# Kernel tuning notes

Measured on AMD Instinct MI355X. Metric: run time of the kernel, lower is better.

## Reference

```python
import jax, jax.numpy as jnp
import numpy as np

N = 100_000      # lidar points (KITTI-scale)
E = 800_000      # knn edges, avg degree 8
C_IN = 4
INTERNAL_H, INTERNAL_W = 240, 1216   # INTERNAL_IMG_SIZE


def setup_inputs() -> dict:
    key = jax.random.key(0)
    ks = jax.random.split(key, 16)
    x = jax.random.normal(ks[0], (N, C_IN), jnp.float32)
    # lidar-like points in velodyne frame: x fwd [5,70], y left [-20,20], z up [-2,1]
    u = jax.random.uniform(ks[1], (N, 3), jnp.float32)
    pos = jnp.stack([5.0 + 65.0 * u[:, 0],
                     -20.0 + 40.0 * u[:, 1],
                     -2.0 + 3.0 * u[:, 2]], axis=1)
    edge_index = jax.random.randint(ks[2], (2, E), 0, N, dtype=jnp.int32)
    batch = jnp.zeros((N,), jnp.int32)
    # folded calibration P2 @ R0 @ Tr: pinhole cam looking down velodyne +x
    f, cx, cy = 720.0, 621.0, 250.0
    proj = jnp.array([[cx, -f, 0.0, 0.0],
                      [cy, 0.0, -f, 0.0],
                      [1.0, 0.0, 0.0, 0.0]], jnp.float32)
    dims = [(C_IN + 3, 64), (64 + 3, 128), (128 + 3, 256)]
    params = {}
    ki = 3
    for li, (din, dout) in enumerate(dims, 1):
        s1, s2 = 1.0 / np.sqrt(din), 1.0 / np.sqrt(dout)
        params[f"w1_{li}"] = jax.random.uniform(ks[ki], (din, dout), jnp.float32, -s1, s1); ki += 1
        params[f"b1_{li}"] = jnp.zeros((dout,), jnp.float32)
        params[f"w2_{li}"] = jax.random.uniform(ks[ki], (dout, dout), jnp.float32, -s2, s2); ki += 1
        params[f"b2_{li}"] = jnp.zeros((dout,), jnp.float32)
    return dict(x=x, pos=pos, edge_index=edge_index, batch=batch, proj=proj,
                img_h=375, img_w=1242, **params)


def _pointnet_conv(x, pos, src, dst, w1, b1, w2, b2):
    # message: local_nn([x_j, pos_j - pos_i]) with MLP = lin1 -> relu -> lin2; aggr = max
    m = jnp.concatenate([x[src], pos[src] - pos[dst]], axis=1)     # [E', din]
    h = jnp.maximum(m @ w1 + b1, 0.0) @ w2 + b2                    # [E', dout]
    return jax.ops.segment_max(h, dst, num_segments=x.shape[0])


def reference(x, pos, edge_index, batch, proj, img_h, img_w,
              w1_1, b1_1, w2_1, b2_1,
              w1_2, b1_2, w2_2, b2_2,
              w1_3, b1_3, w2_3, b2_3):
    n = x.shape[0]
    # PointNetConv adds self-loops by default -> every segment non-empty
    loops = jnp.arange(n, dtype=edge_index.dtype)
    src = jnp.concatenate([edge_index[0], loops])
    dst = jnp.concatenate([edge_index[1], loops])

    h = _pointnet_conv(x, pos, src, dst, w1_1, b1_1, w2_1, b2_1)   # [N, 64]
    h = _pointnet_conv(h, pos, src, dst, w1_2, b1_2, w2_2, b2_2)   # [N, 128]
    h = _pointnet_conv(h, pos, src, dst, w1_3, b1_3, w2_3, b2_3)   # [N, 256]

    # projection: (proj @ [pos; 1]) -> [3, N]; perspective divide; int16 trunc
    hom = proj @ jnp.concatenate([pos.T, jnp.ones((1, n), pos.dtype)], axis=0)
    off_u, off_v = img_w - INTERNAL_W, img_h - INTERNAL_H
    ui = (hom[0] / hom[2]).astype(jnp.int16).astype(jnp.int32) - off_u
    vi = (hom[1] / hom[2]).astype(jnp.int16).astype(jnp.int32) - off_v
    valid = (ui >= 0) & (vi >= 0) & (ui < INTERNAL_W) & (vi < INTERNAL_H)
    # route invalid points out-of-bounds so mode='drop' discards them
    ui = jnp.where(valid, ui, INTERNAL_W)
    vi = jnp.where(valid, vi, INTERNAL_H)

    img = jnp.zeros((1, h.shape[1], INTERNAL_W, INTERNAL_H), h.dtype)  # (B=1, C, 1216, 240)
    img = img.at[0, :, ui, vi].add(h, mode='drop')

    # max_pool2d(kernel=4, stride=4) -> (1, 256, 304, 60)
    B, C, W, H = img.shape
    pooled = img.reshape(B, C, W // 4, 4, H // 4, 4).max(axis=(3, 5))
    return pooled
```

## Files before the change

kernel.cpp:

```cpp
#include <hip/hip_runtime.h>
#include <cstdint>

#define N_PTS 100000
#define N_EDGE 800000
#define N_ITEMS (N_EDGE + N_PTS)
#define IMG_W 1216
#define IMG_H 240
#define OW 304
#define OH 60
#define CHUNK 32
#define BIN_BLOCKS 391

typedef _Float16 f16;
typedef _Float16 f16x8 __attribute__((ext_vector_type(8)));
typedef float f32x4 __attribute__((ext_vector_type(4)));

__device__ __forceinline__ void atomicMaxF(float* addr, float v) {
    if (v >= 0.0f) atomicMax((int*)addr, __float_as_int(v));
    else atomicMin((unsigned int*)addr, __float_as_uint(v));
}

__global__ __launch_bounds__(256)
void init_out_kernel(float* __restrict__ p, long n)
{
    long i = ((long)blockIdx.x * 256 + threadIdx.x) * 4;
    if (i < n) {
        float4 v = {-INFINITY, -INFINITY, -INFINITY, -INFINITY};
        *(float4*)&p[i] = v;
    }
}

template<int DX, int KP, int D>
__global__ __launch_bounds__(256)
void node_mfma_kernel(const float* __restrict__ X, const float* __restrict__ pos,
                      const f16* __restrict__ w1t, const float* __restrict__ b1,
                      f16* __restrict__ A)
{
    constexpr int KB = KP / 32;
    constexpr int NB = D / 16;
    const int tid = threadIdx.x;
    const int wave = tid >> 6;
    const int lane = tid & 63;
    const int row = lane & 15;
    const int kg = lane >> 4;
    const int wbase = (blockIdx.x * 4 + wave) * 32;

    f16x8 pa[2][KB];
#pragma unroll
    for (int mh = 0; mh < 2; ++mh) {
        int n = wbase + mh * 16 + row;
        int ns = (n < N_PTS) ? n : 0;
#pragma unroll
        for (int kb = 0; kb < KB; ++kb) {
            const int c0 = kb * 32 + kg * 8;
            f16x8 h;
#pragma unroll
            for (int j = 0; j < 8; ++j) {
                int k = c0 + j;
                float v = 0.0f;
                if (k < DX) v = X[(long)ns * DX + k];
                else if (k < DX + 3) v = pos[(long)ns * 3 + (k - DX)];
                h[j] = (f16)v;
            }
            pa[mh][kb] = h;
        }
    }

#pragma unroll 2
    for (int nb = 0; nb < NB; ++nb) {
        f32x4 acc0 = {0.0f, 0.0f, 0.0f, 0.0f};
        f32x4 acc1 = {0.0f, 0.0f, 0.0f, 0.0f};
#pragma unroll
        for (int kb = 0; kb < KB; ++kb) {
            f16x8 pb = *(const f16x8*)&w1t[(long)(nb * 16 + row) * KP + kb * 32 + kg * 8];
            acc0 = __builtin_amdgcn_mfma_f32_16x16x32_f16(pa[0][kb], pb, acc0, 0, 0, 0);
            acc1 = __builtin_amdgcn_mfma_f32_16x16x32_f16(pa[1][kb], pb, acc1, 0, 0, 0);
        }
        const int col = nb * 16 + row;
        const float bb = b1[col];
#pragma unroll
        for (int reg = 0; reg < 4; ++reg) {
            int r = kg * 4 + reg;
            int n0 = wbase + r;
            int n1 = wbase + 16 + r;
            if (n0 < N_PTS) A[(long)n0 * D + col] = (f16)(acc0[reg] + bb);
            if (n1 < N_PTS) A[(long)n1 * D + col] = (f16)(acc1[reg] + bb);
        }
    }
}

__global__ void cvt_w1(const float* __restrict__ w1, f16* __restrict__ w1t,
                       int K, int KP, int D)
{
    int i = blockIdx.x * 256 + threadIdx.x;
    if (i >= D * KP) return;
    int c = i / KP, k = i % KP;
    w1t[i] = (k < K) ? (f16)w1[k * D + c] : (f16)0.0f;
}

__global__ void cvt_w2(const float* __restrict__ w2, f16* __restrict__ w2t, int D)
{
    int i = blockIdx.x * 256 + threadIdx.x;
    if (i >= D * D) return;
    int n = i / D, k = i % D;
    w2t[i] = (f16)w2[k * D + n];
}

__global__ void init_hist_kernel(int* __restrict__ hist)
{
    int i = blockIdx.x * 256 + threadIdx.x;
    if (i < N_PTS) hist[i] = 1;
}

__global__ void hist_kernel(const int* __restrict__ ei, int* __restrict__ hist)
{
    int e = blockIdx.x * 256 + threadIdx.x;
    if (e < N_EDGE) atomicAdd(&hist[ei[N_EDGE + e]], 1);
}

__global__ void bsum_kernel(const int* __restrict__ hist, int* __restrict__ bsum)
{
    __shared__ int s[256];
    int i = blockIdx.x * 256 + threadIdx.x;
    s[threadIdx.x] = (i < N_PTS) ? hist[i] : 0;
    __syncthreads();
    for (int off = 128; off > 0; off >>= 1) {
        if (threadIdx.x < off) s[threadIdx.x] += s[threadIdx.x + off];
        __syncthreads();
    }
    if (threadIdx.x == 0) bsum[blockIdx.x] = s[0];
}

__global__ void scan_bsum_kernel(int* __restrict__ bsum)
{
    __shared__ int s[512];
    int t = threadIdx.x;
    int v = (t < BIN_BLOCKS) ? bsum[t] : 0;
    s[t] = v;
    __syncthreads();
    for (int off = 1; off < 512; off <<= 1) {
        int u = (t >= off) ? s[t - off] : 0;
        __syncthreads();
        s[t] += u;
        __syncthreads();
    }
    if (t < BIN_BLOCKS) bsum[t] = s[t] - v;
}

__global__ void rowptr_kernel(const int* __restrict__ hist, const int* __restrict__ bsum,
                              int* __restrict__ woff)
{
    __shared__ int s[256];
    int i = blockIdx.x * 256 + threadIdx.x;
    int v = (i < N_PTS) ? hist[i] : 0;
    s[threadIdx.x] = v;
    __syncthreads();
    for (int off = 1; off < 256; off <<= 1) {
        int u = (threadIdx.x >= off) ? s[threadIdx.x - off] : 0;
        __syncthreads();
        s[threadIdx.x] += u;
        __syncthreads();
    }
    if (i < N_PTS) woff[i] = bsum[blockIdx.x] + s[threadIdx.x] - v;
}

__global__ void scatter_edges_kernel(const int* __restrict__ ei, int* __restrict__ woff,
                                     int* __restrict__ srcS, int* __restrict__ dstS)
{
    int e = blockIdx.x * 256 + threadIdx.x;
    if (e >= N_ITEMS) return;
    int s, d;
    if (e < N_EDGE) { s = ei[e]; d = ei[N_EDGE + e]; }
    else            { s = d = e - N_EDGE; }
    int p = atomicAdd(&woff[d], 1);
    srcS[p] = s;
    dstS[p] = d;
}

template<int D>
__global__ __launch_bounds__(256)
void gemm_msg_kernel(const int* __restrict__ srcA, const int* __restrict__ dstA,
                     const f16* __restrict__ A, const float* __restrict__ pos,
                     const float* __restrict__ w1p, const f16* __restrict__ w2t,
                     const float* __restrict__ b2, float* __restrict__ OUT, int nItems)
{
    constexpr int KB = D / 32;
    constexpr int NB = D / 16;
    const int tid = threadIdx.x;
    const int wave = tid >> 6;
    const int lane = tid & 63;
    const int row = lane & 15;
    const int kg = lane >> 4;
    const long wbase = ((long)blockIdx.x * 4 + wave) * 32;

    int s[2], d[2];
    float px[2], py[2], pz[2];
#pragma unroll
    for (int mh = 0; mh < 2; ++mh) {
        long e = wbase + mh * 16 + row;
        bool ok = (e < nItems);
        int ss = ok ? srcA[e] : 0;
        int dd = ok ? dstA[e] : -1;
        s[mh] = ss; d[mh] = dd;
        int dsafe = ok ? dd : 0;
        px[mh] = pos[(long)dsafe * 3 + 0];
        py[mh] = pos[(long)dsafe * 3 + 1];
        pz[mh] = pos[(long)dsafe * 3 + 2];
    }

    f16x8 pa[2][KB];
#pragma unroll
    for (int kb = 0; kb < KB; ++kb) {
        const int c0 = kb * 32 + kg * 8;
        f16x8 a0 = *(const f16x8*)&A[(long)s[0] * D + c0];
        f16x8 a1 = *(const f16x8*)&A[(long)s[1] * D + c0];
        f16x8 h0, h1;
#pragma unroll
        for (int j = 0; j < 8; ++j) {
            float wx = w1p[c0 + j];
            float wy = w1p[D + c0 + j];
            float wz = w1p[2 * D + c0 + j];
            h0[j] = (f16)fmaxf((float)a0[j] - (px[0] * wx + py[0] * wy + pz[0] * wz), 0.0f);
            h1[j] = (f16)fmaxf((float)a1[j] - (px[1] * wx + py[1] * wy + pz[1] * wz), 0.0f);
        }
        pa[0][kb] = h0;
        pa[1][kb] = h1;
    }

    int dd0[4], dd1[4];
#pragma unroll
    for (int reg = 0; reg < 4; ++reg) {
        int r = kg * 4 + reg;
        dd0[reg] = __shfl(d[0], r);
        dd1[reg] = __shfl(d[1], r);
    }
    const bool a01 = (dd0[1] == dd0[0]), a12 = (dd0[2] == dd0[1]), a23 = (dd0[3] == dd0[2]);
    const bool b01 = (dd1[1] == dd1[0]), b12 = (dd1[2] == dd1[1]), b23 = (dd1[3] == dd1[2]);
    const bool aAll = a01 && a12 && a23, bAll = b01 && b12 && b23;
    const int aN0 = __shfl(dd0[0], lane + 16);
    const int bN0 = __shfl(dd1[0], lane + 16);
    const int aFn = __shfl((int)aAll, lane + 16);
    const int bFn = __shfl((int)bAll, lane + 16);
    const bool aCo = (kg < 3) && (dd0[3] == aN0);
    const bool bCo = (kg < 3) && (dd1[3] == bN0);
    const int lprev = (lane >= 16) ? (lane - 16) : 0;
    const int aP3 = __shfl(dd0[3], lprev);
    const int bP3 = __shfl(dd1[3], lprev);
    const bool aHd = (kg == 0) || (dd0[0] != aP3);
    const bool bHd = (kg == 0) || (dd1[0] != bP3);

#pragma unroll
    for (int nb = 0; nb < NB; ++nb) {
        f32x4 acc0 = {0.0f, 0.0f, 0.0f, 0.0f};
        f32x4 acc1 = {0.0f, 0.0f, 0.0f, 0.0f};
#pragma unroll
        for (int kb = 0; kb < KB; ++kb) {
            f16x8 pb = *(const f16x8*)&w2t[(long)(nb * 16 + row) * D + kb * 32 + kg * 8];
            acc0 = __builtin_amdgcn_mfma_f32_16x16x32_f16(pa[0][kb], pb, acc0, 0, 0, 0);
            acc1 = __builtin_amdgcn_mfma_f32_16x16x32_f16(pa[1][kb], pb, acc1, 0, 0, 0);
        }
        const int col = nb * 16 + row;
        const float bb = b2[col];
        {
            const float v0 = acc0[0] + bb, v1 = acc0[1] + bb, v2 = acc0[2] + bb, v3 = acc0[3] + bb;
            const float s3 = v3;
            const float s2 = a23 ? fmaxf(v2, s3) : v2;
            const float s1 = a12 ? fmaxf(v1, s2) : v1;
            const float s0 = a01 ? fmaxf(v0, s1) : v0;
            float P = v0;
            P = a01 ? fmaxf(P, v1) : P;
            P = (a01 && a12) ? fmaxf(P, v2) : P;
            P = aAll ? fmaxf(P, v3) : P;
            float T = -INFINITY;
#pragma unroll
            for (int it = 0; it < 3; ++it) {
                float Pn = __shfl(P, lane + 16);
                float Tn = __shfl(T, lane + 16);
                T = aCo ? fmaxf(Pn, aFn ? Tn : -INFINITY) : T;
            }
            const float x0 = aAll ? fmaxf(s0, T) : s0;
            const float x1 = (a12 && a23) ? fmaxf(s1, T) : s1;
            const float x2 = a23 ? fmaxf(s2, T) : s2;
            const float x3 = fmaxf(s3, T);
            if (aHd  && dd0[0] >= 0) atomicMaxF(&OUT[(long)dd0[0] * D + col], x0);
            if (!a01 && dd0[1] >= 0) atomicMaxF(&OUT[(long)dd0[1] * D + col], x1);
            if (!a12 && dd0[2] >= 0) atomicMaxF(&OUT[(long)dd0[2] * D + col], x2);
            if (!a23 && dd0[3] >= 0) atomicMaxF(&OUT[(long)dd0[3] * D + col], x3);
        }
        {
            const float v0 = acc1[0] + bb, v1 = acc1[1] + bb, v2 = acc1[2] + bb, v3 = acc1[3] + bb;
            const float s3 = v3;
            const float s2 = b23 ? fmaxf(v2, s3) : v2;
            const float s1 = b12 ? fmaxf(v1, s2) : v1;
            const float s0 = b01 ? fmaxf(v0, s1) : v0;
            float P = v0;
            P = b01 ? fmaxf(P, v1) : P;
            P = (b01 && b12) ? fmaxf(P, v2) : P;
            P = bAll ? fmaxf(P, v3) : P;
            float T = -INFINITY;
#pragma unroll
            for (int it = 0; it < 3; ++it) {
                float Pn = __shfl(P, lane + 16);
                float Tn = __shfl(T, lane + 16);
                T = bCo ? fmaxf(Pn, bFn ? Tn : -INFINITY) : T;
            }
            const float x0 = bAll ? fmaxf(s0, T) : s0;
            const float x1 = (b12 && b23) ? fmaxf(s1, T) : s1;
            const float x2 = b23 ? fmaxf(s2, T) : s2;
            const float x3 = fmaxf(s3, T);
            if (bHd  && dd1[0] >= 0) atomicMaxF(&OUT[(long)dd1[0] * D + col], x0);
            if (!b01 && dd1[1] >= 0) atomicMaxF(&OUT[(long)dd1[1] * D + col], x1);
            if (!b12 && dd1[2] >= 0) atomicMaxF(&OUT[(long)dd1[2] * D + col], x2);
            if (!b23 && dd1[3] >= 0) atomicMaxF(&OUT[(long)dd1[3] * D + col], x3);
        }
    }
}

__global__ void proj_kernel(const float* __restrict__ pos, const float* __restrict__ proj,
                            const int* __restrict__ img_h, const int* __restrict__ img_w,
                            int* __restrict__ pix)
{
    int n = blockIdx.x * blockDim.x + threadIdx.x;
    if (n >= N_PTS) return;
    float px = pos[n * 3 + 0], py = pos[n * 3 + 1], pz = pos[n * 3 + 2];
    float h0 = proj[0] * px + proj[1] * py + proj[2]  * pz + proj[3];
    float h1 = proj[4] * px + proj[5] * py + proj[6]  * pz + proj[7];
    float h2 = proj[8] * px + proj[9] * py + proj[10] * pz + proj[11];
    int off_u = img_w[0] - IMG_W;
    int off_v = img_h[0] - IMG_H;
    int ui = (int)(short)(h0 / h2) - off_u;
    int vi = (int)(short)(h1 / h2) - off_v;
    bool valid = (ui >= 0) && (vi >= 0) && (ui < IMG_W) && (vi < IMG_H);
    pix[n] = valid ? (ui * IMG_H + vi) : -1;
}

__global__ __launch_bounds__(256)
void scatter_kernel(const float* __restrict__ H, const int* __restrict__ pix,
                    float* __restrict__ img, int cbase)
{
    long g = (long)blockIdx.x * blockDim.x + threadIdx.x;
    if (g >= (long)N_PTS * CHUNK) return;
    int n = (int)(g / CHUNK);
    int c = (int)(g % CHUNK);
    int p = pix[n];
    if (p < 0) return;
    atomicAdd(&img[(long)p * CHUNK + c], H[(long)n * 256 + cbase + c]);
}

__global__ __launch_bounds__(CHUNK)
void pool_kernel(const float* __restrict__ img, float* __restrict__ out, int cbase)
{
    int cell = blockIdx.x;
    int wc = cell / OH, hc = cell % OH;
    int c = threadIdx.x;
    float mx = -INFINITY;
#pragma unroll
    for (int i = 0; i < 4; ++i)
#pragma unroll
        for (int j = 0; j < 4; ++j) {
            long p = (long)(wc * 4 + i) * IMG_H + (hc * 4 + j);
            mx = fmaxf(mx, img[p * CHUNK + c]);
        }
    out[(long)(cbase + c) * (OW * OH) + wc * OH + hc] = mx;
}

extern "C" void kernel_launch(void* const* d_in, const int* in_sizes, int n_in,
                              void* d_out, int out_size, void* d_ws, size_t ws_size,
                              hipStream_t stream)
{
    const float* x     = (const float*)d_in[0];
    const float* pos   = (const float*)d_in[1];
    const int*   ei    = (const int*)d_in[2];
    const float* proj  = (const float*)d_in[4];
    const int*   img_h = (const int*)d_in[5];
    const int*   img_w = (const int*)d_in[6];
    const float* w1_1 = (const float*)d_in[7];
    const float* b1_1 = (const float*)d_in[8];
    const float* w2_1 = (const float*)d_in[9];
    const float* b2_1 = (const float*)d_in[10];
    const float* w1_2 = (const float*)d_in[11];
    const float* b1_2 = (const float*)d_in[12];
    const float* w2_2 = (const float*)d_in[13];
    const float* b2_2 = (const float*)d_in[14];
    const float* w1_3 = (const float*)d_in[15];
    const float* b1_3 = (const float*)d_in[16];
    const float* w2_3 = (const float*)d_in[17];
    const float* b2_3 = (const float*)d_in[18];
    float* out = (float*)d_out;

    if (ws_size < 162400000ull) return;
    char* ws = (char*)d_ws;
    float* HH   = (float*)(ws + 0);
    float* F1   = (float*)(ws + 0);
    float* F0   = (float*)(ws + 51200000);
    f16*   A12  = (f16*)(ws + 76800000);
    f16*   A3   = (f16*)(ws + 102400000);
    float* img  = (float*)(ws + 102400000);
    int*   pix  = (int*)(ws + 153600000);
    f16*   w2t3 = (f16*)(ws + 154000000);
    f16*   w2t2 = (f16*)(ws + 154131072);
    f16*   w2t1 = (f16*)(ws + 154163840);
    int*   srcS = (int*)(ws + 154200000);
    int*   dstS = (int*)(ws + 157800000);
    int*   hist = (int*)(ws + 161400000);
    int*   woff = (int*)(ws + 161800000);
    int*   bsum = (int*)(ws + 162200000);
    f16*   w1t3 = (f16*)(ws + 162210000);
    f16*   w1t2 = (f16*)(ws + 162300000);
    f16*   w1t1 = (f16*)(ws + 162330000);

    const int NODE_BLOCKS = (N_PTS + 127) / 128;
    const int EDGE_BLOCKS = (N_ITEMS + 127) / 128;
    const int E256  = (N_EDGE + 255) / 256;
    const int I256  = (N_ITEMS + 255) / 256;

    init_hist_kernel<<<BIN_BLOCKS, 256, 0, stream>>>(hist);
    hist_kernel<<<E256, 256, 0, stream>>>(ei, hist);
    bsum_kernel<<<BIN_BLOCKS, 256, 0, stream>>>(hist, bsum);
    scan_bsum_kernel<<<1, 512, 0, stream>>>(bsum);
    rowptr_kernel<<<BIN_BLOCKS, 256, 0, stream>>>(hist, bsum, woff);
    scatter_edges_kernel<<<I256, 256, 0, stream>>>(ei, woff, srcS, dstS);

    cvt_w1<<<(64 * 32 + 255) / 256, 256, 0, stream>>>(w1_1, w1t1, 7, 32, 64);
    cvt_w1<<<(128 * 96 + 255) / 256, 256, 0, stream>>>(w1_2, w1t2, 67, 96, 128);
    cvt_w1<<<(256 * 160 + 255) / 256, 256, 0, stream>>>(w1_3, w1t3, 131, 160, 256);
    cvt_w2<<<(64 * 64 + 255) / 256, 256, 0, stream>>>(w2_1, w2t1, 64);
    cvt_w2<<<(128 * 128 + 255) / 256, 256, 0, stream>>>(w2_2, w2t2, 128);
    cvt_w2<<<(256 * 256 + 255) / 256, 256, 0, stream>>>(w2_3, w2t3, 256);
    proj_kernel<<<(N_PTS + 255) / 256, 256, 0, stream>>>(pos, proj, img_h, img_w, pix);
    init_out_kernel<<<(N_PTS * 64 / 4 + 255) / 256, 256, 0, stream>>>(F0, (long)N_PTS * 64);
    init_out_kernel<<<(N_PTS * 128 / 4 + 255) / 256, 256, 0, stream>>>(F1, (long)N_PTS * 128);

    node_mfma_kernel<4, 32, 64><<<NODE_BLOCKS, 256, 0, stream>>>(x, pos, w1t1, b1_1, A12);
    gemm_msg_kernel<64><<<EDGE_BLOCKS, 256, 0, stream>>>(srcS, dstS, A12, pos, w1_1 + 4 * 64, w2t1, b2_1, F0, N_ITEMS);

    node_mfma_kernel<64, 96, 128><<<NODE_BLOCKS, 256, 0, stream>>>(F0, pos, w1t2, b1_2, A12);
    gemm_msg_kernel<128><<<EDGE_BLOCKS, 256, 0, stream>>>(srcS, dstS, A12, pos, w1_2 + 64 * 128, w2t2, b2_2, F1, N_ITEMS);

    node_mfma_kernel<128, 160, 256><<<NODE_BLOCKS, 256, 0, stream>>>(F1, pos, w1t3, b1_3, A3);
    init_out_kernel<<<(N_PTS * 256 / 4 + 255) / 256, 256, 0, stream>>>(HH, (long)N_PTS * 256);
    gemm_msg_kernel<256><<<EDGE_BLOCKS, 256, 0, stream>>>(srcS, dstS, A3, pos, w1_3 + 128 * 256, w2t3, b2_3, HH, N_ITEMS);

    for (int cb = 0; cb < 256; cb += CHUNK) {
        hipMemsetAsync(img, 0, (size_t)IMG_W * IMG_H * CHUNK * 4, stream);
        scatter_kernel<<<(N_PTS * CHUNK) / 256, 256, 0, stream>>>(HH, pix, img, cb);
        pool_kernel<<<OW * OH, CHUNK, 0, stream>>>(img, out, cb);
    }
}
```

Before: 1.735 ms.

## Use 16-edge-per-wave MFMA message kernel for layer 3

Adds a variant of the edge message kernel where each wave handles 16 edges instead of 32, keeping the first-layer activations in registers and running 16x16x32 MFMAs over the 256-wide output. It is used only for the third PointNet layer, where the D=256 tile likely causes register pressure and low occupancy. The trade is more blocks and twice as many loads of W2 per edge, in exchange for fewer registers per wave and possibly higher occupancy.

```diff
diff --git a/kernel.cpp b/kernel.cpp
--- a/kernel.cpp
+++ b/kernel.cpp
@@ -313,6 +313,96 @@
             if (!b12 && dd1[2] >= 0) atomicMaxF(&OUT[(long)dd1[2] * D + col], x2);
             if (!b23 && dd1[3] >= 0) atomicMaxF(&OUT[(long)dd1[3] * D + col], x3);
         }
+    }
+}
+
+template<int D>
+__global__ __launch_bounds__(256)
+void gemm_msg16_kernel(const int* __restrict__ srcA, const int* __restrict__ dstA,
+                       const f16* __restrict__ A, const float* __restrict__ pos,
+                       const float* __restrict__ w1p, const f16* __restrict__ w2t,
+                       const float* __restrict__ b2, float* __restrict__ OUT, int nItems)
+{
+    constexpr int KB = D / 32;
+    constexpr int NB = D / 16;
+    const int tid = threadIdx.x;
+    const int wave = tid >> 6;
+    const int lane = tid & 63;
+    const int row = lane & 15;
+    const int kg = lane >> 4;
+    const long wbase = ((long)blockIdx.x * 4 + wave) * 16;
+
+    const long e = wbase + row;
+    const bool ok = (e < nItems);
+    const int ss = ok ? srcA[e] : 0;
+    const int dd = ok ? dstA[e] : -1;
+    const int dsafe = ok ? dd : 0;
+    const float px = pos[(long)dsafe * 3 + 0];
+    const float py = pos[(long)dsafe * 3 + 1];
+    const float pz = pos[(long)dsafe * 3 + 2];
+
+    f16x8 pa[KB];
+#pragma unroll
+    for (int kb = 0; kb < KB; ++kb) {
+        const int c0 = kb * 32 + kg * 8;
+        f16x8 a = *(const f16x8*)&A[(long)ss * D + c0];
+        f16x8 h;
+#pragma unroll
+        for (int j = 0; j < 8; ++j) {
+            float wx = w1p[c0 + j];
+            float wy = w1p[D + c0 + j];
+            float wz = w1p[2 * D + c0 + j];
+            h[j] = (f16)fmaxf((float)a[j] - (px * wx + py * wy + pz * wz), 0.0f);
+        }
+        pa[kb] = h;
+    }
+
+    int dd0[4];
+#pragma unroll
+    for (int reg = 0; reg < 4; ++reg) dd0[reg] = __shfl(dd, kg * 4 + reg);
+    const bool a01 = (dd0[1] == dd0[0]), a12 = (dd0[2] == dd0[1]), a23 = (dd0[3] == dd0[2]);
+    const bool aAll = a01 && a12 && a23;
+    const int aN0 = __shfl(dd0[0], lane + 16);
+    const int aFn = __shfl((int)aAll, lane + 16);
+    const bool aCo = (kg < 3) && (dd0[3] == aN0);
+    const int lprev = (lane >= 16) ? (lane - 16) : 0;
+    const int aP3 = __shfl(dd0[3], lprev);
+    const bool aHd = (kg == 0) || (dd0[0] != aP3);
+
+#pragma unroll
+    for (int nb = 0; nb < NB; ++nb) {
+        f32x4 acc = {0.0f, 0.0f, 0.0f, 0.0f};
+#pragma unroll
+        for (int kb = 0; kb < KB; ++kb) {
+            f16x8 pb = *(const f16x8*)&w2t[(long)(nb * 16 + row) * D + kb * 32 + kg * 8];
+            acc = __builtin_amdgcn_mfma_f32_16x16x32_f16(pa[kb], pb, acc, 0, 0, 0);
+        }
+        const int col = nb * 16 + row;
+        const float bb = b2[col];
+        const float v0 = acc[0] + bb, v1 = acc[1] + bb, v2 = acc[2] + bb, v3 = acc[3] + bb;
+        const float s3 = v3;
+        const float s2 = a23 ? fmaxf(v2, s3) : v2;
+        const float s1 = a12 ? fmaxf(v1, s2) : v1;
+        const float s0 = a01 ? fmaxf(v0, s1) : v0;
+        float P = v0;
+        P = a01 ? fmaxf(P, v1) : P;
+        P = (a01 && a12) ? fmaxf(P, v2) : P;
+        P = aAll ? fmaxf(P, v3) : P;
+        float T = -INFINITY;
+#pragma unroll
+        for (int it = 0; it < 3; ++it) {
+            float Pn = __shfl(P, lane + 16);
+            float Tn = __shfl(T, lane + 16);
+            T = aCo ? fmaxf(Pn, aFn ? Tn : -INFINITY) : T;
+        }
+        const float x0 = aAll ? fmaxf(s0, T) : s0;
+        const float x1 = (a12 && a23) ? fmaxf(s1, T) : s1;
+        const float x2 = a23 ? fmaxf(s2, T) : s2;
+        const float x3 = fmaxf(s3, T);
+        if (aHd  && dd0[0] >= 0) atomicMaxF(&OUT[(long)dd0[0] * D + col], x0);
+        if (!a01 && dd0[1] >= 0) atomicMaxF(&OUT[(long)dd0[1] * D + col], x1);
+        if (!a12 && dd0[2] >= 0) atomicMaxF(&OUT[(long)dd0[2] * D + col], x2);
+        if (!a23 && dd0[3] >= 0) atomicMaxF(&OUT[(long)dd0[3] * D + col], x3);
     }
 }
 
@@ -409,8 +499,9 @@
     f16*   w1t2 = (f16*)(ws + 162300000);
     f16*   w1t1 = (f16*)(ws + 162330000);
 
-    const int NODE_BLOCKS = (N_PTS + 127) / 128;
-    const int EDGE_BLOCKS = (N_ITEMS + 127) / 128;
+    const int NODE_BLOCKS  = (N_PTS + 127) / 128;
+    const int EDGE_BLOCKS  = (N_ITEMS + 127) / 128;
+    const int EDGE16_BLOCKS = (N_ITEMS + 63) / 64;
     const int E256  = (N_EDGE + 255) / 256;
     const int I256  = (N_ITEMS + 255) / 256;
 
@@ -439,7 +530,7 @@
 
     node_mfma_kernel<128, 160, 256><<<NODE_BLOCKS, 256, 0, stream>>>(F1, pos, w1t3, b1_3, A3);
     init_out_kernel<<<(N_PTS * 256 / 4 + 255) / 256, 256, 0, stream>>>(HH, (long)N_PTS * 256);
-    gemm_msg_kernel<256><<<EDGE_BLOCKS, 256, 0, stream>>>(srcS, dstS, A3, pos, w1_3 + 128 * 256, w2t3, b2_3, HH, N_ITEMS);
+    gemm_msg16_kernel<256><<<EDGE16_BLOCKS, 256, 0, stream>>>(srcS, dstS, A3, pos, w1_3 + 128 * 256, w2t3, b2_3, HH, N_ITEMS);
 
     for (int cb = 0; cb < 256; cb += CHUNK) {
         hipMemsetAsync(img, 0, (size_t)IMG_W * IMG_H * CHUNK * 4, stream);
```

Result: slower. 1.783 ms (+2.8%).
